# Kernel tuning notes

Measured on AMD Instinct MI355X. Metric: run time of the kernel, lower is better.

The kernel has to match this reference:

```python
import jax, jax.numpy as jnp
import numpy as np

N, E = 50000, 800000
IN_DIM, HEADS, OUT_DIM = 128, 4, 32
NEG_SLOPE = 0.2
EPS = 1e-16


def setup_inputs() -> dict:
    key = jax.random.key(0)
    k = jax.random.split(key, 6)
    x = jax.random.normal(k[0], (N, IN_DIM), dtype=jnp.float32)
    edge_index = jax.random.randint(k[1], (2, E), 0, N, dtype=jnp.int64)
    # xavier-uniform-ish params
    lim_w = float(np.sqrt(6.0 / (IN_DIM + HEADS * OUT_DIM)))
    W = jax.random.uniform(k[2], (HEADS * OUT_DIM, IN_DIM), minval=-lim_w, maxval=lim_w, dtype=jnp.float32)
    lim_a = float(np.sqrt(6.0 / (1 + HEADS * OUT_DIM)))
    att_src = jax.random.uniform(k[3], (1, HEADS, OUT_DIM), minval=-lim_a, maxval=lim_a, dtype=jnp.float32)
    att_dst = jax.random.uniform(k[4], (1, HEADS, OUT_DIM), minval=-lim_a, maxval=lim_a, dtype=jnp.float32)
    bias = jnp.zeros((HEADS * OUT_DIM,), dtype=jnp.float32)
    return {"x": x, "edge_index": edge_index, "W": W, "att_src": att_src, "att_dst": att_dst, "bias": bias}


def reference(x, edge_index, W, att_src, att_dst, bias):
    n = x.shape[0]
    h = (x @ W.T).reshape(n, HEADS, OUT_DIM)           # (N,H,D)
    src, dst = edge_index[0], edge_index[1]
    a_src = jnp.sum(h * att_src, axis=-1)              # (N,H)
    a_dst = jnp.sum(h * att_dst, axis=-1)              # (N,H)
    alpha = a_src[src] + a_dst[dst]                    # (E,H)
    alpha = jax.nn.leaky_relu(alpha, NEG_SLOPE)
    # segment (per-dst) softmax over edges, per head
    m = jax.ops.segment_max(alpha, dst, num_segments=n)   # (N,H)
    ex = jnp.exp(alpha - m[dst])
    s = jax.ops.segment_sum(ex, dst, num_segments=n)      # (N,H)
    alpha = ex / (s[dst] + EPS)                            # (E,H)
    # dropout p=0 (eval) -> identity
    msg = h[src] * alpha[..., None]                        # (E,H,D)
    out = jax.ops.segment_sum(msg, dst, num_segments=n)    # (N,H,D)
    out = out.reshape(n, HEADS * OUT_DIM) + bias
    alpha_pooled = alpha.mean(axis=-1)                     # (E,)
    return out, alpha_pooled
```

## Files before the change

kernel.cpp:

```cpp
#include <hip/hip_runtime.h>

#define NNODES 50000
#define NEDGES 800000
#define HD 128
#define NEG 0.2f
#define MTILE 64
#define LDW 136
#define GEMMB ((NNODES + MTILE - 1) / MTILE)
#define NBINS 196
#define CAP 5120
#define GST 16
#define ABLK ((NEDGES + 2047) / 2048)
#define ECAP 1536

typedef __attribute__((ext_vector_type(8))) short short8;
typedef __attribute__((ext_vector_type(4))) float floatx4;

static __device__ inline unsigned short f2bf(float f) {
    unsigned u = __float_as_uint(f);
    return (unsigned short)((u + 0x7FFF + ((u >> 16) & 1)) >> 16);
}
static __device__ inline float bf2f(unsigned short u) {
    return __uint_as_float(((unsigned)u) << 16);
}
static __device__ inline float lrelu_exp(float a) {
    a = (a > 0.f) ? a : NEG * a;
    return __expf(a);
}

__global__ __launch_bounds__(256, 4) void gat_main(
    const float* __restrict__ x, const float* __restrict__ W,
    const float* __restrict__ att_src, const float* __restrict__ att_dst,
    const int* __restrict__ ei,
    unsigned short* __restrict__ h, float* __restrict__ asrc,
    float* __restrict__ adst, int* __restrict__ gcnt, int* __restrict__ cbuf)
{
    __shared__ unsigned short Wl[128 * LDW];
    const int t = threadIdx.x;

    if (blockIdx.x >= GEMMB) {
        int* hist = (int*)Wl;
        int* boff = hist + 256;
        const int e0 = (blockIdx.x - GEMMB) * 2048 + t * 8;
        const bool act = (e0 < NEDGES);
        int4 s0 = make_int4(0, 0, 0, 0), s1 = s0, d0 = s0, d1 = s0;
        if (act) {
            s0 = *(const int4*)(ei + e0);
            s1 = *(const int4*)(ei + e0 + 4);
            d0 = *(const int4*)(ei + NEDGES + e0);
            d1 = *(const int4*)(ei + NEDGES + e0 + 4);
        }
        hist[t] = 0;
        __syncthreads();
        if (act) {
            atomicAdd(&hist[d0.x >> 8], 1); atomicAdd(&hist[d0.y >> 8], 1);
            atomicAdd(&hist[d0.z >> 8], 1); atomicAdd(&hist[d0.w >> 8], 1);
            atomicAdd(&hist[d1.x >> 8], 1); atomicAdd(&hist[d1.y >> 8], 1);
            atomicAdd(&hist[d1.z >> 8], 1); atomicAdd(&hist[d1.w >> 8], 1);
        }
        __syncthreads();
        if (t < NBINS && hist[t] > 0)
            boff[t] = atomicAdd(&gcnt[t * GST], hist[t]);
        __syncthreads();
        if (act) {
            int ss[8] = {s0.x, s0.y, s0.z, s0.w, s1.x, s1.y, s1.z, s1.w};
            int dd[8] = {d0.x, d0.y, d0.z, d0.w, d1.x, d1.y, d1.z, d1.w};
#pragma unroll
            for (int j = 0; j < 8; j++) {
                int b = dd[j] >> 8;
                int slot = atomicAdd(&boff[b], 1);
                cbuf[(size_t)b * CAP + slot] = ((dd[j] & 255) << 16) | ss[j];
            }
        }
        return;
    }

    const int rowBase = blockIdx.x * MTILE;

    for (int idx = t * 8; idx < 128 * 128; idx += 2048) {
        int r = idx >> 7, c = idx & 127;
        float4 v0 = *(const float4*)(W + idx);
        float4 v1 = *(const float4*)(W + idx + 4);
        short8 u;
        u[0] = (short)f2bf(v0.x); u[1] = (short)f2bf(v0.y);
        u[2] = (short)f2bf(v0.z); u[3] = (short)f2bf(v0.w);
        u[4] = (short)f2bf(v1.x); u[5] = (short)f2bf(v1.y);
        u[6] = (short)f2bf(v1.z); u[7] = (short)f2bf(v1.w);
        *(short8*)(Wl + r * LDW + c) = u;
    }

    const int wave = t >> 6;
    const int lane = t & 63;
    const int c16  = lane & 15;
    const int quad = lane >> 4;
    const int xr   = rowBase + wave * 16 + c16;
    short8 av[4];
#pragma unroll
    for (int kc = 0; kc < 4; kc++) {
        float4 v0 = make_float4(0.f, 0.f, 0.f, 0.f);
        float4 v1 = v0;
        if (xr < NNODES) {
            const float* p = x + (size_t)xr * 128 + kc * 32 + quad * 8;
            v0 = *(const float4*)p;
            v1 = *(const float4*)(p + 4);
        }
        short8 u;
        u[0] = (short)f2bf(v0.x); u[1] = (short)f2bf(v0.y);
        u[2] = (short)f2bf(v0.z); u[3] = (short)f2bf(v0.w);
        u[4] = (short)f2bf(v1.x); u[5] = (short)f2bf(v1.y);
        u[6] = (short)f2bf(v1.z); u[7] = (short)f2bf(v1.w);
        av[kc] = u;
    }
    __syncthreads();

    floatx4 acc[8];
#pragma unroll
    for (int nt = 0; nt < 8; nt++) acc[nt] = (floatx4)(0.f);

#pragma unroll
    for (int kc = 0; kc < 4; kc++) {
#pragma unroll
        for (int nt = 0; nt < 8; nt++) {
            short8 bv = *(const short8*)(Wl + (nt * 16 + c16) * LDW + kc * 32 + quad * 8);
            acc[nt] = __builtin_amdgcn_mfma_f32_16x16x32_bf16(av[kc], bv, acc[nt], 0, 0, 0);
        }
    }

    float As[8], Ad[8];
#pragma unroll
    for (int nt = 0; nt < 8; nt++) {
        As[nt] = att_src[nt * 16 + c16];
        Ad[nt] = att_dst[nt * 16 + c16];
    }
#pragma unroll
    for (int r = 0; r < 4; r++) {
        const int gr = rowBase + wave * 16 + quad * 4 + r;
#pragma unroll
        for (int hh = 0; hh < 4; hh++) {
            float ps = acc[2 * hh][r] * As[2 * hh] + acc[2 * hh + 1][r] * As[2 * hh + 1];
            float pd = acc[2 * hh][r] * Ad[2 * hh] + acc[2 * hh + 1][r] * Ad[2 * hh + 1];
#pragma unroll
            for (int m = 8; m >= 1; m >>= 1) {
                ps += __shfl_xor(ps, m, 64);
                pd += __shfl_xor(pd, m, 64);
            }
            if (c16 == 0 && gr < NNODES) {
                asrc[gr * 4 + hh] = ps;
                adst[gr * 4 + hh] = pd;
            }
        }
    }

    __syncthreads();
#pragma unroll
    for (int r = 0; r < 4; r++) {
        const int lr = wave * 16 + quad * 4 + r;
#pragma unroll
        for (int nt = 0; nt < 8; nt++)
            Wl[lr * LDW + nt * 16 + c16] = f2bf(acc[nt][r]);
    }
    __syncthreads();
    for (int idx = t * 8; idx < MTILE * 128; idx += 2048) {
        int r = idx >> 7, c = idx & 127;
        int g = rowBase + r;
        if (g < NNODES)
            *(short8*)(h + (size_t)g * HD + c) = *(const short8*)(Wl + r * LDW + c);
    }
}

__global__ __launch_bounds__(256) void gat_fuse(
    const int* __restrict__ gcnt, const int* __restrict__ cbuf,
    const float* __restrict__ asrc, const float* __restrict__ adst,
    const unsigned short* __restrict__ h, const float* __restrict__ bias,
    float* __restrict__ out, float* __restrict__ rsumr)
{
    __shared__ unsigned short eb[ECAP];
    __shared__ float sh_w[ECAP * 4];
    __shared__ int hist[64], run[64], beg[65];
    const int t = threadIdx.x;
    const int b = blockIdx.x >> 2;
    const int q = blockIdx.x & 3;
    const int c_b = gcnt[b * GST];
    const size_t wbase = (size_t)b * CAP;

    if (t < 64) hist[t] = 0;
    __syncthreads();
    for (int i = t; i < c_b; i += 256) {
        int e = cbuf[wbase + i];
        int f = (e >> 16) & 255;
        if ((f >> 6) == q) atomicAdd(&hist[f & 63], 1);
    }
    __syncthreads();
    if (t < 64) {
        int v = hist[t];
        int s = v;
#pragma unroll
        for (int off = 1; off < 64; off <<= 1) {
            int u = __shfl_up(s, off, 64);
            if (t >= off) s += u;
        }
        beg[t] = s - v;
        run[t] = s - v;
        if (t == 63) beg[64] = s;
    }
    __syncthreads();
    for (int i = t; i < c_b; i += 256) {
        int e = cbuf[wbase + i];
        int f = (e >> 16) & 255;
        if ((f >> 6) == q) {
            int slot = atomicAdd(&run[f & 63], 1);
            if (slot < ECAP) eb[slot] = (unsigned short)(e & 0xFFFF);
        }
    }
    __syncthreads();

    const int grp  = t >> 5;
    const int k    = t & 31;
    const int head = k >> 3;
    const float4 bias4 = *(const float4*)(bias + k * 4);

    for (int ii = 0; ii < 8; ii++) {
        const int local = grp * 8 + ii;
        const int n = b * 256 + q * 64 + local;
        int eB = beg[local], eE = beg[local + 1];
        if (eE > ECAP) eE = ECAP;
        if (eB > ECAP) eB = ECAP;

        float4 bn = make_float4(0.f, 0.f, 0.f, 0.f);
        if (n < NNODES) bn = *(const float4*)(adst + n * 4);

        float4 sum = make_float4(0.f, 0.f, 0.f, 0.f);
        for (int j = eB + k; j < eE; j += 32) {
            int s = eb[j];
            float4 a = *(const float4*)(asrc + s * 4);
            float4 wv;
            wv.x = lrelu_exp(a.x + bn.x);
            wv.y = lrelu_exp(a.y + bn.y);
            wv.z = lrelu_exp(a.z + bn.z);
            wv.w = lrelu_exp(a.w + bn.w);
            sum.x += wv.x; sum.y += wv.y; sum.z += wv.z; sum.w += wv.w;
            *(float4*)(sh_w + j * 4) = wv;
        }
#pragma unroll
        for (int m = 16; m >= 1; m >>= 1) {
            sum.x += __shfl_xor(sum.x, m, 64);
            sum.y += __shfl_xor(sum.y, m, 64);
            sum.z += __shfl_xor(sum.z, m, 64);
            sum.w += __shfl_xor(sum.w, m, 64);
        }
        float rs[4];
        rs[0] = 1.f / (sum.x + 1e-16f);
        rs[1] = 1.f / (sum.y + 1e-16f);
        rs[2] = 1.f / (sum.z + 1e-16f);
        rs[3] = 1.f / (sum.w + 1e-16f);
        if (n < NNODES && k == 0) {
            float4 r4 = make_float4(rs[0], rs[1], rs[2], rs[3]);
            *(float4*)(rsumr + n * 4) = r4;
        }
        const float rsel = rs[head];

        float4 acc = bias4;
        float4 acc2 = make_float4(0.f, 0.f, 0.f, 0.f);
        int i = eB;
        for (; i + 4 <= eE; i += 4) {
            int s0 = eb[i];
            int s1 = eb[i + 1];
            int s2 = eb[i + 2];
            int s3 = eb[i + 3];
            float w0 = sh_w[i * 4 + head] * rsel;
            float w1 = sh_w[(i + 1) * 4 + head] * rsel;
            float w2 = sh_w[(i + 2) * 4 + head] * rsel;
            float w3 = sh_w[(i + 3) * 4 + head] * rsel;
            ushort4 u0 = *(const ushort4*)(h + (size_t)s0 * HD + k * 4);
            ushort4 u1 = *(const ushort4*)(h + (size_t)s1 * HD + k * 4);
            ushort4 u2 = *(const ushort4*)(h + (size_t)s2 * HD + k * 4);
            ushort4 u3 = *(const ushort4*)(h + (size_t)s3 * HD + k * 4);
            acc.x  = fmaf(bf2f(u0.x), w0, acc.x);
            acc.y  = fmaf(bf2f(u0.y), w0, acc.y);
            acc.z  = fmaf(bf2f(u0.z), w0, acc.z);
            acc.w  = fmaf(bf2f(u0.w), w0, acc.w);
            acc2.x = fmaf(bf2f(u1.x), w1, acc2.x);
            acc2.y = fmaf(bf2f(u1.y), w1, acc2.y);
            acc2.z = fmaf(bf2f(u1.z), w1, acc2.z);
            acc2.w = fmaf(bf2f(u1.w), w1, acc2.w);
            acc.x  = fmaf(bf2f(u2.x), w2, acc.x);
            acc.y  = fmaf(bf2f(u2.y), w2, acc.y);
            acc.z  = fmaf(bf2f(u2.z), w2, acc.z);
            acc.w  = fmaf(bf2f(u2.w), w2, acc.w);
            acc2.x = fmaf(bf2f(u3.x), w3, acc2.x);
            acc2.y = fmaf(bf2f(u3.y), w3, acc2.y);
            acc2.z = fmaf(bf2f(u3.z), w3, acc2.z);
            acc2.w = fmaf(bf2f(u3.w), w3, acc2.w);
        }
        for (; i < eE; i++) {
            int s0 = eb[i];
            float w0 = sh_w[i * 4 + head] * rsel;
            ushort4 u0 = *(const ushort4*)(h + (size_t)s0 * HD + k * 4);
            acc.x = fmaf(bf2f(u0.x), w0, acc.x);
            acc.y = fmaf(bf2f(u0.y), w0, acc.y);
            acc.z = fmaf(bf2f(u0.z), w0, acc.z);
            acc.w = fmaf(bf2f(u0.w), w0, acc.w);
        }
        acc.x += acc2.x; acc.y += acc2.y; acc.z += acc2.z; acc.w += acc2.w;
        if (n < NNODES)
            *(float4*)(out + (size_t)n * HD + k * 4) = acc;
    }
}

static __device__ inline float apool1(
    int s, int d, const float* __restrict__ asrc,
    const float* __restrict__ adst, const float* __restrict__ rsumr)
{
    float4 a = *(const float4*)(asrc + s * 4);
    float4 b = *(const float4*)(adst + d * 4);
    float4 r = *(const float4*)(rsumr + d * 4);
    return 0.25f * (lrelu_exp(a.x + b.x) * r.x + lrelu_exp(a.y + b.y) * r.y +
                    lrelu_exp(a.z + b.z) * r.z + lrelu_exp(a.w + b.w) * r.w);
}

__global__ __launch_bounds__(256) void gat_apool(
    const int* __restrict__ ei, const float* __restrict__ asrc,
    const float* __restrict__ adst, const float* __restrict__ rsumr,
    float* __restrict__ apool)
{
    int e0 = (blockIdx.x * 256 + threadIdx.x) * 4;
    if (e0 >= NEDGES) return;
    int4 s = *(const int4*)(ei + e0);
    int4 d = *(const int4*)(ei + NEDGES + e0);
    float4 r;
    r.x = apool1(s.x, d.x, asrc, adst, rsumr);
    r.y = apool1(s.y, d.y, asrc, adst, rsumr);
    r.z = apool1(s.z, d.z, asrc, adst, rsumr);
    r.w = apool1(s.w, d.w, asrc, adst, rsumr);
    *(float4*)(apool + e0) = r;
}

extern "C" void kernel_launch(void* const* d_in, const int* in_sizes, int n_in,
                              void* d_out, int out_size, void* d_ws, size_t ws_size,
                              hipStream_t stream)
{
    const float* x       = (const float*)d_in[0];
    const int*   ei      = (const int*)d_in[1];
    const float* W       = (const float*)d_in[2];
    const float* att_src = (const float*)d_in[3];
    const float* att_dst = (const float*)d_in[4];
    const float* bias    = (const float*)d_in[5];

    float* out   = (float*)d_out;
    float* apool = out + (size_t)NNODES * HD;

    unsigned short* h = (unsigned short*)d_ws;
    float* asrc  = (float*)(h + (size_t)NNODES * HD);
    float* adst  = asrc + NNODES * 4;
    float* rsumr = adst + NNODES * 4;
    int*   gcnt  = (int*)(rsumr + NNODES * 4);
    int*   cbuf  = gcnt + NBINS * GST;

    hipMemsetAsync(gcnt, 0, (size_t)NBINS * GST * sizeof(int), stream);

    gat_main<<<GEMMB + ABLK, 256, 0, stream>>>(
        x, W, att_src, att_dst, ei, h, asrc, adst, gcnt, cbuf);
    gat_fuse<<<NBINS * 4, 256, 0, stream>>>(
        gcnt, cbuf, asrc, adst, h, bias, out, rsumr);
    gat_apool<<<(NEDGES / 4 + 255) / 256, 256, 0, stream>>>(
        ei, asrc, adst, rsumr, apool);
}
```

Baseline: 166.5 us.

## Split fused bin/aggregate kernel into CSR build plus per-node gather kernel

Replaces the fused kernel, which re-scanned each bin's edges four times, with a dedicated binning kernel. That kernel builds a global CSR (per-node offsets plus a compacted source array) once per bin. A new per-node kernel then uses one 32-lane group per node, with 8 nodes per block and 6250 blocks. It caches up to 64 edge weights in shared memory and gathers h rows with wider 16-byte loads split across two half-groups, reducing them with a shuffle. This adds a kernel launch and an extra global round-trip for the CSR, but removes the redundant scans, the large shared-memory footprint and the ECAP truncation.

Measured after the change: 167.7 us. About the same (+0.7%).

```diff
diff --git a/kernel.cpp b/kernel.cpp
--- a/kernel.cpp
+++ b/kernel.cpp
@@ -6,12 +6,12 @@
 #define NEG 0.2f
 #define MTILE 64
 #define LDW 136
+#define MAXD 64
 #define GEMMB ((NNODES + MTILE - 1) / MTILE)
 #define NBINS 196
 #define CAP 5120
 #define GST 16
 #define ABLK ((NEDGES + 2047) / 2048)
-#define ECAP 1536
 
 typedef __attribute__((ext_vector_type(8))) short short8;
 typedef __attribute__((ext_vector_type(4))) float floatx4;
@@ -168,143 +168,182 @@
     }
 }
 
-__global__ __launch_bounds__(256) void gat_fuse(
+__global__ __launch_bounds__(1024) void gat_bin(
     const int* __restrict__ gcnt, const int* __restrict__ cbuf,
+    int* __restrict__ coff, unsigned short* __restrict__ csr)
+{
+    __shared__ unsigned short eb[CAP];
+    __shared__ int sh[256], hist[256], run[256];
+    const int t = threadIdx.x;
+    const int b = blockIdx.x;
+    const int c_b = gcnt[b * GST];
+    const size_t wbase = (size_t)b * CAP;
+
+    if (t < 256) {
+        sh[t] = (t < NBINS) ? gcnt[t * GST] : 0;
+        hist[t] = 0;
+    }
+    __syncthreads();
+    for (int off = 1; off < 256; off <<= 1) {
+        int u = (t < 256 && t >= off) ? sh[t - off] : 0;
+        __syncthreads();
+        if (t < 256) sh[t] += u;
+        __syncthreads();
+    }
+    const int binbase = sh[b] - c_b;
+
+    for (int i = t; i < c_b; i += 1024)
+        atomicAdd(&hist[(cbuf[wbase + i] >> 16) & 255], 1);
+    __syncthreads();
+
+    int hv = 0;
+    if (t < 256) { hv = hist[t]; sh[t] = hv; }
+    __syncthreads();
+    for (int off = 1; off < 256; off <<= 1) {
+        int u = (t < 256 && t >= off) ? sh[t - off] : 0;
+        __syncthreads();
+        if (t < 256) sh[t] += u;
+        __syncthreads();
+    }
+    if (t < 256) {
+        int ex = sh[t] - hv;
+        int n = b * 256 + t;
+        if (n < NNODES) coff[n] = binbase + ex;
+        run[t] = ex;
+    }
+    if (b == 0 && t == 0) coff[NNODES] = NEDGES;
+    __syncthreads();
+
+    for (int i = t; i < c_b; i += 1024) {
+        int e = cbuf[wbase + i];
+        int slot = atomicAdd(&run[(e >> 16) & 255], 1);
+        eb[slot] = (unsigned short)(e & 0xFFFF);
+    }
+    __syncthreads();
+
+    for (int i = t; i < c_b; i += 1024)
+        csr[binbase + i] = eb[i];
+}
+
+__global__ __launch_bounds__(256) void gat_node(
+    const int* __restrict__ coff, const unsigned short* __restrict__ csr,
     const float* __restrict__ asrc, const float* __restrict__ adst,
     const unsigned short* __restrict__ h, const float* __restrict__ bias,
     float* __restrict__ out, float* __restrict__ rsumr)
 {
-    __shared__ unsigned short eb[ECAP];
-    __shared__ float sh_w[ECAP * 4];
-    __shared__ int hist[64], run[64], beg[65];
+    __shared__ unsigned short sh_src[8 * MAXD];
+    __shared__ float sh_w[8 * MAXD * 4];
     const int t = threadIdx.x;
-    const int b = blockIdx.x >> 2;
-    const int q = blockIdx.x & 3;
-    const int c_b = gcnt[b * GST];
-    const size_t wbase = (size_t)b * CAP;
-
-    if (t < 64) hist[t] = 0;
-    __syncthreads();
-    for (int i = t; i < c_b; i += 256) {
-        int e = cbuf[wbase + i];
-        int f = (e >> 16) & 255;
-        if ((f >> 6) == q) atomicAdd(&hist[f & 63], 1);
-    }
-    __syncthreads();
-    if (t < 64) {
-        int v = hist[t];
-        int s = v;
-#pragma unroll
-        for (int off = 1; off < 64; off <<= 1) {
-            int u = __shfl_up(s, off, 64);
-            if (t >= off) s += u;
-        }
-        beg[t] = s - v;
-        run[t] = s - v;
-        if (t == 63) beg[64] = s;
-    }
-    __syncthreads();
-    for (int i = t; i < c_b; i += 256) {
-        int e = cbuf[wbase + i];
-        int f = (e >> 16) & 255;
-        if ((f >> 6) == q) {
-            int slot = atomicAdd(&run[f & 63], 1);
-            if (slot < ECAP) eb[slot] = (unsigned short)(e & 0xFFFF);
-        }
-    }
-    __syncthreads();
-
-    const int grp  = t >> 5;
-    const int k    = t & 31;
-    const int head = k >> 3;
-    const float4 bias4 = *(const float4*)(bias + k * 4);
-
-    for (int ii = 0; ii < 8; ii++) {
-        const int local = grp * 8 + ii;
-        const int n = b * 256 + q * 64 + local;
-        int eB = beg[local], eE = beg[local + 1];
-        if (eE > ECAP) eE = ECAP;
-        if (eB > ECAP) eB = ECAP;
-
-        float4 bn = make_float4(0.f, 0.f, 0.f, 0.f);
-        if (n < NNODES) bn = *(const float4*)(adst + n * 4);
-
-        float4 sum = make_float4(0.f, 0.f, 0.f, 0.f);
-        for (int j = eB + k; j < eE; j += 32) {
-            int s = eb[j];
-            float4 a = *(const float4*)(asrc + s * 4);
-            float4 wv;
-            wv.x = lrelu_exp(a.x + bn.x);
-            wv.y = lrelu_exp(a.y + bn.y);
-            wv.z = lrelu_exp(a.z + bn.z);
-            wv.w = lrelu_exp(a.w + bn.w);
-            sum.x += wv.x; sum.y += wv.y; sum.z += wv.z; sum.w += wv.w;
-            *(float4*)(sh_w + j * 4) = wv;
-        }
-#pragma unroll
-        for (int m = 16; m >= 1; m >>= 1) {
-            sum.x += __shfl_xor(sum.x, m, 64);
-            sum.y += __shfl_xor(sum.y, m, 64);
-            sum.z += __shfl_xor(sum.z, m, 64);
-            sum.w += __shfl_xor(sum.w, m, 64);
-        }
-        float rs[4];
-        rs[0] = 1.f / (sum.x + 1e-16f);
-        rs[1] = 1.f / (sum.y + 1e-16f);
-        rs[2] = 1.f / (sum.z + 1e-16f);
-        rs[3] = 1.f / (sum.w + 1e-16f);
-        if (n < NNODES && k == 0) {
-            float4 r4 = make_float4(rs[0], rs[1], rs[2], rs[3]);
-            *(float4*)(rsumr + n * 4) = r4;
-        }
-        const float rsel = rs[head];
-
-        float4 acc = bias4;
-        float4 acc2 = make_float4(0.f, 0.f, 0.f, 0.f);
-        int i = eB;
-        for (; i + 4 <= eE; i += 4) {
-            int s0 = eb[i];
-            int s1 = eb[i + 1];
-            int s2 = eb[i + 2];
-            int s3 = eb[i + 3];
-            float w0 = sh_w[i * 4 + head] * rsel;
-            float w1 = sh_w[(i + 1) * 4 + head] * rsel;
-            float w2 = sh_w[(i + 2) * 4 + head] * rsel;
-            float w3 = sh_w[(i + 3) * 4 + head] * rsel;
-            ushort4 u0 = *(const ushort4*)(h + (size_t)s0 * HD + k * 4);
-            ushort4 u1 = *(const ushort4*)(h + (size_t)s1 * HD + k * 4);
-            ushort4 u2 = *(const ushort4*)(h + (size_t)s2 * HD + k * 4);
-            ushort4 u3 = *(const ushort4*)(h + (size_t)s3 * HD + k * 4);
-            acc.x  = fmaf(bf2f(u0.x), w0, acc.x);
-            acc.y  = fmaf(bf2f(u0.y), w0, acc.y);
-            acc.z  = fmaf(bf2f(u0.z), w0, acc.z);
-            acc.w  = fmaf(bf2f(u0.w), w0, acc.w);
-            acc2.x = fmaf(bf2f(u1.x), w1, acc2.x);
-            acc2.y = fmaf(bf2f(u1.y), w1, acc2.y);
-            acc2.z = fmaf(bf2f(u1.z), w1, acc2.z);
-            acc2.w = fmaf(bf2f(u1.w), w1, acc2.w);
-            acc.x  = fmaf(bf2f(u2.x), w2, acc.x);
-            acc.y  = fmaf(bf2f(u2.y), w2, acc.y);
-            acc.z  = fmaf(bf2f(u2.z), w2, acc.z);
-            acc.w  = fmaf(bf2f(u2.w), w2, acc.w);
-            acc2.x = fmaf(bf2f(u3.x), w3, acc2.x);
-            acc2.y = fmaf(bf2f(u3.y), w3, acc2.y);
-            acc2.z = fmaf(bf2f(u3.z), w3, acc2.z);
-            acc2.w = fmaf(bf2f(u3.w), w3, acc2.w);
-        }
-        for (; i < eE; i++) {
-            int s0 = eb[i];
-            float w0 = sh_w[i * 4 + head] * rsel;
-            ushort4 u0 = *(const ushort4*)(h + (size_t)s0 * HD + k * 4);
-            acc.x = fmaf(bf2f(u0.x), w0, acc.x);
-            acc.y = fmaf(bf2f(u0.y), w0, acc.y);
-            acc.z = fmaf(bf2f(u0.z), w0, acc.z);
-            acc.w = fmaf(bf2f(u0.w), w0, acc.w);
-        }
-        acc.x += acc2.x; acc.y += acc2.y; acc.z += acc2.z; acc.w += acc2.w;
-        if (n < NNODES)
-            *(float4*)(out + (size_t)n * HD + k * 4) = acc;
-    }
+    const int node8 = t >> 5;
+    const int n = blockIdx.x * 8 + node8;
+    const int k = t & 31;
+    const int beg = coff[n], end = coff[n + 1];
+    const int base = node8 * MAXD;
+    const float4 bn = *(const float4*)(adst + n * 4);
+
+    float4 sum = make_float4(0.f, 0.f, 0.f, 0.f);
+    for (int j = beg + k; j < end; j += 32) {
+        int s = csr[j];
+        float4 a = *(const float4*)(asrc + s * 4);
+        float4 wv;
+        wv.x = lrelu_exp(a.x + bn.x);
+        wv.y = lrelu_exp(a.y + bn.y);
+        wv.z = lrelu_exp(a.z + bn.z);
+        wv.w = lrelu_exp(a.w + bn.w);
+        sum.x += wv.x; sum.y += wv.y; sum.z += wv.z; sum.w += wv.w;
+        int i = j - beg;
+        if (i < MAXD) {
+            sh_src[base + i] = (unsigned short)s;
+            *(float4*)(sh_w + (base + i) * 4) = wv;
+        }
+    }
+#pragma unroll
+    for (int m = 16; m >= 1; m >>= 1) {
+        sum.x += __shfl_xor(sum.x, m, 64);
+        sum.y += __shfl_xor(sum.y, m, 64);
+        sum.z += __shfl_xor(sum.z, m, 64);
+        sum.w += __shfl_xor(sum.w, m, 64);
+    }
+    float rs[4];
+    rs[0] = 1.f / (sum.x + 1e-16f);
+    rs[1] = 1.f / (sum.y + 1e-16f);
+    rs[2] = 1.f / (sum.z + 1e-16f);
+    rs[3] = 1.f / (sum.w + 1e-16f);
+    if (k == 0)
+        *(float4*)(rsumr + n * 4) = make_float4(rs[0], rs[1], rs[2], rs[3]);
+
+    const int half = k >> 4;
+    const int i16  = k & 15;
+    const int head = i16 >> 2;
+    const float rsel = rs[head];
+    const int lim = (end - beg < MAXD) ? end - beg : MAXD;
+
+    float accA[8], accB[8];
+#pragma unroll
+    for (int m = 0; m < 8; m++) { accA[m] = 0.f; accB[m] = 0.f; }
+
+    int j = 0;
+    for (; j + 8 <= lim; j += 8) {
+        int e0 = j + half, e1 = j + 2 + half, e2 = j + 4 + half, e3 = j + 6 + half;
+        int s0 = sh_src[base + e0];
+        int s1 = sh_src[base + e1];
+        int s2 = sh_src[base + e2];
+        int s3 = sh_src[base + e3];
+        float w0 = sh_w[(base + e0) * 4 + head] * rsel;
+        float w1 = sh_w[(base + e1) * 4 + head] * rsel;
+        float w2 = sh_w[(base + e2) * 4 + head] * rsel;
+        float w3 = sh_w[(base + e3) * 4 + head] * rsel;
+        short8 u0 = *(const short8*)(h + (size_t)s0 * HD + i16 * 8);
+        short8 u1 = *(const short8*)(h + (size_t)s1 * HD + i16 * 8);
+        short8 u2 = *(const short8*)(h + (size_t)s2 * HD + i16 * 8);
+        short8 u3 = *(const short8*)(h + (size_t)s3 * HD + i16 * 8);
+#pragma unroll
+        for (int m = 0; m < 8; m++) {
+            accA[m] = fmaf(bf2f((unsigned short)u0[m]), w0, accA[m]);
+            accB[m] = fmaf(bf2f((unsigned short)u1[m]), w1, accB[m]);
+            accA[m] = fmaf(bf2f((unsigned short)u2[m]), w2, accA[m]);
+            accB[m] = fmaf(bf2f((unsigned short)u3[m]), w3, accB[m]);
+        }
+    }
+    for (; j + 2 <= lim; j += 2) {
+        int e0 = j + half;
+        int s0 = sh_src[base + e0];
+        float w0 = sh_w[(base + e0) * 4 + head] * rsel;
+        short8 u0 = *(const short8*)(h + (size_t)s0 * HD + i16 * 8);
+#pragma unroll
+        for (int m = 0; m < 8; m++)
+            accA[m] = fmaf(bf2f((unsigned short)u0[m]), w0, accA[m]);
+    }
+    if (j < lim && half == 0) {
+        int s0 = sh_src[base + j];
+        float w0 = sh_w[(base + j) * 4 + head] * rsel;
+        short8 u0 = *(const short8*)(h + (size_t)s0 * HD + i16 * 8);
+#pragma unroll
+        for (int m = 0; m < 8; m++)
+            accA[m] = fmaf(bf2f((unsigned short)u0[m]), w0, accA[m]);
+    }
+    const float bnh = ((const float*)&bn)[head];
+    for (int jj = beg + MAXD + half; jj < end; jj += 2) {
+        int s0 = csr[jj];
+        float w0 = lrelu_exp(asrc[s0 * 4 + head] + bnh) * rsel;
+        short8 u0 = *(const short8*)(h + (size_t)s0 * HD + i16 * 8);
+#pragma unroll
+        for (int m = 0; m < 8; m++)
+            accA[m] = fmaf(bf2f((unsigned short)u0[m]), w0, accA[m]);
+    }
+
+#pragma unroll
+    for (int m = 0; m < 8; m++) {
+        accA[m] += accB[m];
+        accA[m] += __shfl_xor(accA[m], 16, 64);
+    }
+    const float4 b4 = *(const float4*)(bias + i16 * 8 + half * 4);
+    float4 st;
+    st.x = accA[half * 4 + 0] + b4.x;
+    st.y = accA[half * 4 + 1] + b4.y;
+    st.z = accA[half * 4 + 2] + b4.z;
+    st.w = accA[half * 4 + 3] + b4.w;
+    *(float4*)(out + (size_t)n * HD + i16 * 8 + half * 4) = st;
 }
 
 static __device__ inline float apool1(
@@ -354,14 +393,17 @@
     float* adst  = asrc + NNODES * 4;
     float* rsumr = adst + NNODES * 4;
     int*   gcnt  = (int*)(rsumr + NNODES * 4);
-    int*   cbuf  = gcnt + NBINS * GST;
+    int*   coff  = gcnt + NBINS * GST;
+    int*   cbuf  = coff + NNODES + 4;
+    unsigned short* csr = (unsigned short*)(cbuf + (size_t)NBINS * CAP);
 
     hipMemsetAsync(gcnt, 0, (size_t)NBINS * GST * sizeof(int), stream);
 
     gat_main<<<GEMMB + ABLK, 256, 0, stream>>>(
         x, W, att_src, att_dst, ei, h, asrc, adst, gcnt, cbuf);
-    gat_fuse<<<NBINS * 4, 256, 0, stream>>>(
-        gcnt, cbuf, asrc, adst, h, bias, out, rsumr);
+    gat_bin<<<NBINS, 1024, 0, stream>>>(gcnt, cbuf, coff, csr);
+    gat_node<<<NNODES / 8, 256, 0, stream>>>(
+        coff, csr, asrc, adst, h, bias, out, rsumr);
     gat_apool<<<(NEDGES / 4 + 255) / 256, 256, 0, stream>>>(
         ei, asrc, adst, rsumr, apool);
 }
```
